# Optimization experiments

Hardware: AMD Instinct MI355X
Metric: run time of the kernel (lower is better)

The kernel has to match this reference:

```python
import jax, jax.numpy as jnp
import numpy as np

B, T, D = 2, 1024, 1024   # batch, timesteps (same for src/aux), model_dim
H, HD = 16, 64            # num_heads, head_dim (attention_dim = H*HD = 1024)
F = 4096                  # feedforward_dim
A = H * HD                # attention_dim
SCALE = float(HD) ** 0.5
LN_EPS = 1e-5
MASK_FILL = 1e-32         # faithful to masked_fill(1 - mask, 1e-32)


def setup_inputs() -> dict:
    key = jax.random.key(0)
    ks = jax.random.split(key, 12)
    def w(k, shape, fan):
        return jax.random.normal(k, shape, jnp.float32) / np.sqrt(fan)
    return {
        "src": jax.random.normal(ks[0], (B, T, D), jnp.float32),
        "aux": jax.random.normal(ks[1], (B, T, D), jnp.float32),
        "Wu": w(ks[2], (D, 3 * A), D), "bu": jnp.zeros((3 * A,), jnp.float32),
        "Wv": w(ks[3], (D, 3 * A), D), "bv": jnp.zeros((3 * A,), jnp.float32),
        "Wo": w(ks[4], (A, D), A),     "bo": jnp.zeros((D,), jnp.float32),
        "W1": w(ks[5], (D, F), D),     "b1": jnp.zeros((F,), jnp.float32),
        "W2": w(ks[6], (F, D), F),     "b2": jnp.zeros((D,), jnp.float32),
        "g1": jnp.ones((D,), jnp.float32), "be1": jnp.zeros((D,), jnp.float32),
        "g2": jnp.ones((D,), jnp.float32), "be2": jnp.zeros((D,), jnp.float32),
        "src_mask": jax.random.randint(ks[7], (B, T), 0, 2, jnp.int32),
        "aux_mask": jax.random.randint(ks[8], (B, T), 0, 2, jnp.int32),
    }


def _heads(x):
    # [B, T, A] -> [B, H, T, HD]
    b, t, _ = x.shape
    return x.reshape(b, t, H, HD).transpose(0, 2, 1, 3)


def _merge(x):
    # [B, H, T, HD] -> [B, T, A]
    b, h, t, hd = x.shape
    return x.transpose(0, 2, 1, 3).reshape(b, t, h * hd)


def _layernorm(x, g, b):
    m = jnp.mean(x, axis=-1, keepdims=True)
    v = jnp.var(x, axis=-1, keepdims=True)
    return (x - m) * jax.lax.rsqrt(v + LN_EPS) * g + b


def reference(src, aux, Wu, bu, Wv, bv, Wo, bo, W1, b1, W2, b2,
              g1, be1, g2, be2, src_mask, aux_mask):
    # dual-stream QKV projections
    q_u, k_u, v_u = (_heads(t) for t in jnp.split(src @ Wu + bu, 3, axis=-1))
    q_v, k_v, v_v = (_heads(t) for t in jnp.split(aux @ Wv + bv, 3, axis=-1))

    # masked scaled similarities (masked entries filled with 1e-32, per original)
    sim1 = jnp.einsum('bhqd,bhkd->bhqk', q_u / SCALE, k_v)        # [B,H,T1,T2]
    sim1 = jnp.where(aux_mask[:, None, None, :] > 0, sim1, MASK_FILL)
    sim2 = jnp.einsum('bhqd,bhkd->bhqk', q_v / SCALE, k_u)        # [B,H,T2,T1]
    sim2 = jnp.where(src_mask[:, None, None, :] > 0, sim2, MASK_FILL)

    # combined double-bmm attention
    comb_u = jnp.einsum('bhij,bhjk->bhik', sim1, sim2)            # [B,H,T1,T1]
    att_u = jax.nn.softmax(comb_u, axis=-1)
    out_u = _merge(jnp.einsum('bhqk,bhkd->bhqd', att_u, v_u)) @ Wo + bo

    comb_v = jnp.einsum('bhij,bhjk->bhik', sim2, sim1)            # [B,H,T2,T2]
    att_v = jax.nn.softmax(comb_v, axis=-1)
    out_v = _merge(jnp.einsum('bhqk,bhkd->bhqd', att_v, v_v)) @ Wo + bo

    def second_stage(x, attn):
        o1 = _layernorm(x + attn, g1, be1)
        ffn = jax.nn.relu(o1 @ W1 + b1) @ W2 + b2
        return _layernorm(o1 + ffn, g2, be2)

    return second_stage(src, out_u), second_stage(aux, out_v)
```

## Files before the change

### kernel.cpp

```cpp
#include <hip/hip_runtime.h>
#include <stdint.h>

typedef unsigned short u16;
typedef __attribute__((ext_vector_type(4))) float f32x4;
typedef __attribute__((ext_vector_type(8))) __bf16 bf16x8;
typedef __attribute__((ext_vector_type(8))) unsigned short u16x8;

#define T_ 1024
#define D_ 1024
#define HD_ 64

__device__ __forceinline__ float b2f(u16 u) {
    union { unsigned int i; float f; } x; x.i = ((unsigned int)u) << 16; return x.f;
}
__device__ __forceinline__ u16 f2b(float f) {
    union { float f; unsigned int i; } x; x.f = f;
    unsigned int i = x.i;
    unsigned int r = (i >> 16) & 1;
    i += 0x7fffu + r;
    return (u16)(i >> 16);
}

__device__ __forceinline__ void gl2lds16(const void* g, void* l) {
    auto gp = (const __attribute__((address_space(1))) unsigned int*)(unsigned long long)(g);
    auto lp = (__attribute__((address_space(3))) unsigned int*)(unsigned int)(unsigned long long)(l);
    __builtin_amdgcn_global_load_lds(gp, lp, 16, 0, 0);
}

__device__ __forceinline__ float wred_sum(float v) {
    #pragma unroll
    for (int o = 32; o > 0; o >>= 1) v += __shfl_down(v, o, 64);
    return v;
}
__device__ __forceinline__ float shx(float v, int m) { return __shfl_xor(v, m, 64); }

__global__ __launch_bounds__(256) void transpose_cvt(const float* __restrict__ in,
                                                     u16* __restrict__ out, int R, int C) {
    __shared__ float Ts[64][65];
    int c0 = blockIdx.x * 64, r0 = blockIdx.y * 64;
    int tid = threadIdx.x, tx = tid & 63, ty = tid >> 6;
    #pragma unroll
    for (int i = ty; i < 64; i += 4) Ts[i][tx] = in[(long)(r0 + i) * C + c0 + tx];
    __syncthreads();
    #pragma unroll
    for (int i = ty; i < 64; i += 4)
        out[(long)(c0 + i) * R + r0 + tx] = f2b(Ts[tx][i]);
}

__global__ __launch_bounds__(256) void transpose_split(const float* __restrict__ in,
                                                       u16* __restrict__ out, int R, int C) {
    __shared__ float Ts[64][65];
    int c0 = blockIdx.x * 64, r0 = blockIdx.y * 64;
    int tid = threadIdx.x, tx = tid & 63, ty = tid >> 6;
    #pragma unroll
    for (int i = ty; i < 64; i += 4) Ts[i][tx] = in[(long)(r0 + i) * C + c0 + tx];
    __syncthreads();
    #pragma unroll
    for (int i = ty; i < 64; i += 4) {
        float v = Ts[tx][i];
        u16 hi = f2b(v);
        u16 lo = f2b(v - b2f(hi));
        long base = (long)(c0 + i) * (3 * R) + r0 + tx;
        out[base] = hi;
        out[base + R] = hi;
        out[base + 2 * R] = lo;
    }
}

__global__ __launch_bounds__(256) void split_rows(const float* __restrict__ in,
                                                  u16* __restrict__ out) {
    long row = blockIdx.x;
    int tid = threadIdx.x;
    #pragma unroll
    for (int k = 0; k < 4; k++) {
        int c = tid + k * 256;
        float v = in[row * 1024 + c];
        u16 hi = f2b(v);
        u16 lo = f2b(v - b2f(hi));
        out[row * 3072 + c] = hi;
        out[row * 3072 + 1024 + c] = lo;
        out[row * 3072 + 2048 + c] = hi;
    }
}

enum { EPI_F32_BIAS = 0, EPI_BF16_BIAS = 1, EPI_BF16_BIAS_RELU = 2 };

template <int EPI, int BN>
__global__ __launch_bounds__(256) void gemm128(
    const u16* __restrict__ A, const u16* __restrict__ B, void* __restrict__ C,
    const float* __restrict__ bias,
    int M, int N, int K, int lda, int ldb, int ldc,
    long sAz, long sBz, long sCz) {
    __shared__ u16 As[2][128 * 32];
    __shared__ u16 Bs[2][BN * 32];
    const int tid = threadIdx.x, wave = tid >> 6, lane = tid & 63;
    const int m0 = blockIdx.x * 128, n0 = blockIdx.y * BN;
    const int z = blockIdx.z;
    const u16* Ab = A + (long)z * sAz;
    const u16* Bb = B + (long)z * sBz;
    const int srow = lane >> 2, scol = (lane & 3) * 8;
    constexpr int IT = (BN == 128) ? 4 : 2;
    f32x4 acc[IT][4];
    #pragma unroll
    for (int i = 0; i < IT; i++)
        #pragma unroll
        for (int j = 0; j < 4; j++) acc[i][j] = (f32x4){0.f, 0.f, 0.f, 0.f};
    const int wm = (BN == 128) ? (wave >> 1) * 64 : wave * 32;
    const int wn = (BN == 128) ? (wave & 1) * 64 : 0;
    const int fr = lane & 15, fk = (lane >> 4) * 8;

    {
        #pragma unroll
        for (int t = 0; t < 2; t++) {
            int rb = wave * 32 + t * 16;
            gl2lds16(Ab + (long)(m0 + rb + srow) * lda + scol, &As[0][rb * 32]);
        }
        if constexpr (BN == 128) {
            #pragma unroll
            for (int t = 0; t < 2; t++) {
                int rb = wave * 32 + t * 16;
                gl2lds16(Bb + (long)(n0 + rb + srow) * ldb + scol, &Bs[0][rb * 32]);
            }
        } else {
            int rb = wave * 16;
            gl2lds16(Bb + (long)(n0 + rb + srow) * ldb + scol, &Bs[0][rb * 32]);
        }
    }
    __syncthreads();

    for (int k0 = 0; k0 < K; k0 += 32) {
        const int buf = (k0 >> 5) & 1;
        const int kn = k0 + 32;
        if (kn < K) {
            #pragma unroll
            for (int t = 0; t < 2; t++) {
                int rb = wave * 32 + t * 16;
                gl2lds16(Ab + (long)(m0 + rb + srow) * lda + kn + scol, &As[buf ^ 1][rb * 32]);
            }
            if constexpr (BN == 128) {
                #pragma unroll
                for (int t = 0; t < 2; t++) {
                    int rb = wave * 32 + t * 16;
                    gl2lds16(Bb + (long)(n0 + rb + srow) * ldb + kn + scol, &Bs[buf ^ 1][rb * 32]);
                }
            } else {
                int rb = wave * 16;
                gl2lds16(Bb + (long)(n0 + rb + srow) * ldb + kn + scol, &Bs[buf ^ 1][rb * 32]);
            }
        }
        bf16x8 af[IT], bv[4];
        #pragma unroll
        for (int i = 0; i < IT; i++) af[i] = *(const bf16x8*)&As[buf][(wm + i * 16 + fr) * 32 + fk];
        #pragma unroll
        for (int j = 0; j < 4; j++) bv[j] = *(const bf16x8*)&Bs[buf][(wn + j * 16 + fr) * 32 + fk];
        #pragma unroll
        for (int i = 0; i < IT; i++)
            #pragma unroll
            for (int j = 0; j < 4; j++)
                acc[i][j] = __builtin_amdgcn_mfma_f32_16x16x32_bf16(af[i], bv[j], acc[i][j], 0, 0, 0);
        __syncthreads();
    }
    const int er = (lane >> 4) * 4, ec = lane & 15;
    #pragma unroll
    for (int i = 0; i < IT; i++)
        #pragma unroll
        for (int j = 0; j < 4; j++)
            #pragma unroll
            for (int r = 0; r < 4; r++) {
                const int gm = m0 + wm + i * 16 + er + r;
                const int gn = n0 + wn + j * 16 + ec;
                const float v = acc[i][j][r];
                if constexpr (EPI == EPI_F32_BIAS) {
                    ((float*)C)[(long)z * sCz + (long)gm * ldc + gn] = v + bias[gn];
                } else if constexpr (EPI == EPI_BF16_BIAS) {
                    ((u16*)C)[(long)z * sCz + (long)gm * ldc + gn] = f2b(v + bias[gn]);
                } else {
                    ((u16*)C)[(long)z * sCz + (long)gm * ldc + gn] = f2b(fmaxf(v + bias[gn], 0.0f));
                }
            }
}

__global__ __launch_bounds__(256) void repack_vt(const float* __restrict__ Uf,
                                                 const float* __restrict__ Vf,
                                                 u16* __restrict__ Vt) {
    __shared__ u16 Ts[64][65];
    int tid = threadIdx.x, tx = tid & 63, ty = tid >> 6;
    int t0 = blockIdx.x * 64;
    int sz = blockIdx.y, s = sz >> 5, z = sz & 31, b = z >> 4, h = z & 15;
    const float* srcp = s ? Vf : Uf;
    #pragma unroll
    for (int i = ty; i < 64; i += 4)
        Ts[i][tx] = f2b(srcp[(long)(b * T_ + t0 + i) * 3072 + 2048 + h * 64 + tx]);
    __syncthreads();
    u16* dst = Vt + (long)sz * HD_ * T_;
    #pragma unroll
    for (int i = ty; i < 64; i += 4) dst[(long)i * T_ + t0 + tx] = Ts[tx][i];
}

__global__ __launch_bounds__(256) void rs_part(const float* __restrict__ Uf,
                                               const float* __restrict__ Vf,
                                               const int* __restrict__ smask,
                                               const int* __restrict__ amask,
                                               float* __restrict__ RSp) {
    __shared__ float Ksh[64 * 64];
    __shared__ float Qsh[64 * 64];
    int idx = blockIdx.x;
    int mat = idx >> 5, z = idx & 31, b = z >> 4, h = z & 15;
    int chunk = blockIdx.y, j0 = chunk * 64;
    const float* base = mat ? Uf : Vf;
    const int* mk = mat ? smask : amask;
    int tid = threadIdx.x;
    float4* K4 = (float4*)Ksh;
    float4* Q4 = (float4*)Qsh;
    for (int ii = tid; ii < 1024; ii += 256) {
        int j = ii >> 4, d4 = ii & 15;
        long row = (long)(b * T_ + j0 + j) * 3072 + h * 64;
        int m = mk[b * T_ + j0 + j];
        float4 kv = ((const float4*)&base[row + 1024])[d4];
        if (m <= 0) kv = (float4){0.f, 0.f, 0.f, 0.f};
        K4[ii] = kv;
        Q4[ii] = ((const float4*)&base[row])[d4];
    }
    __syncthreads();
    int d1 = tid >> 2, c0 = (tid & 3) * 16;
    float4 a[4];
    #pragma unroll
    for (int k = 0; k < 4; k++) a[k] = (float4){0.f, 0.f, 0.f, 0.f};
    for (int j = 0; j < 64; j++) {
        float kv = Ksh[j * 64 + d1];
        const float4* q = (const float4*)&Qsh[j * 64 + c0];
        #pragma unroll
        for (int k = 0; k < 4; k++) {
            float4 qv = q[k];
            a[k].x += kv * qv.x; a[k].y += kv * qv.y;
            a[k].z += kv * qv.z; a[k].w += kv * qv.w;
        }
    }
    float4* out = (float4*)&RSp[((long)chunk * 64 + idx) * 4096 + d1 * 64 + c0];
    #pragma unroll
    for (int k = 0; k < 4; k++) out[k] = a[k];
}

__global__ __launch_bounds__(256) void rs_reduce(const float* __restrict__ RSp,
                                                 float* __restrict__ RS) {
    int gid = blockIdx.x * 256 + threadIdx.x;
    const float4* in = (const float4*)RSp;
    float4 s = (float4){0.f, 0.f, 0.f, 0.f};
    #pragma unroll
    for (int c = 0; c < 16; c++) {
        float4 v = in[(long)c * 65536 + gid];
        s.x += v.x; s.y += v.y; s.z += v.z; s.w += v.w;
    }
    ((float4*)RS)[gid] = s;
}

__global__ __launch_bounds__(256) void qprime(const float* __restrict__ Uf,
                                              const float* __restrict__ Vf,
                                              const float* __restrict__ RS,
                                              u16* __restrict__ Qs) {
    __shared__ float Rm[4096];
    __shared__ float Qsh[128][65];
    int t0 = blockIdx.x * 128;
    int sz = blockIdx.y, s = sz >> 5, z = sz & 31, b = z >> 4, h = z & 15;
    const float* Qf = s ? Vf : Uf;
    const float* mat = RS + (long)(s * 32 + z) * 4096;
    int tid = threadIdx.x;
    for (int ii = tid; ii < 1024; ii += 256)
        ((float4*)Rm)[ii] = ((const float4*)mat)[ii];
    for (int ii = tid; ii < 2048; ii += 256) {
        int j = ii >> 4, d4 = ii & 15;
        float4 v = ((const float4*)&Qf[(long)(b * T_ + t0 + j) * 3072 + h * 64])[d4];
        Qsh[j][d4 * 4] = v.x; Qsh[j][d4 * 4 + 1] = v.y;
        Qsh[j][d4 * 4 + 2] = v.z; Qsh[j][d4 * 4 + 3] = v.w;
    }
    __syncthreads();
    int r = tid >> 1, c0 = (tid & 1) * 32;
    float4 acc[8];
    #pragma unroll
    for (int k = 0; k < 8; k++) acc[k] = (float4){0.f, 0.f, 0.f, 0.f};
    for (int d1 = 0; d1 < 64; d1++) {
        float q = Qsh[r][d1];
        const float4* rm = (const float4*)&Rm[d1 * 64 + c0];
        #pragma unroll
        for (int k = 0; k < 8; k++) {
            float4 rv = rm[k];
            acc[k].x += q * rv.x; acc[k].y += q * rv.y;
            acc[k].z += q * rv.z; acc[k].w += q * rv.w;
        }
    }
    u16 hiA[32], loA[32];
    #pragma unroll
    for (int k = 0; k < 8; k++) {
        #pragma unroll
        for (int e = 0; e < 4; e++) {
            float x = ((const float*)&acc[k])[e] * (1.f / 64.f);
            int c = k * 4 + e;
            u16 hi = f2b(x);
            hiA[c] = hi;
            loA[c] = f2b(x - b2f(hi));
        }
    }
    u16* out = Qs + ((long)sz * T_ + (t0 + r)) * 128;
    #pragma unroll
    for (int i = 0; i < 4; i++) {
        *(u16x8*)&out[c0 + i * 8]      = *(const u16x8*)&hiA[i * 8];
        *(u16x8*)&out[64 + c0 + i * 8] = *(const u16x8*)&loA[i * 8];
    }
}

__global__ __launch_bounds__(256) void ksplit(const float* __restrict__ Uf,
                                              const float* __restrict__ Vf,
                                              const int* __restrict__ src_mask,
                                              const int* __restrict__ aux_mask,
                                              u16* __restrict__ Ks) {
    int t0 = blockIdx.x * 64;
    int sz = blockIdx.y, s = sz >> 5, z = sz & 31, b = z >> 4, h = z & 15;
    const float* Kf = s ? Vf : Uf;
    const int* mk = s ? aux_mask : src_mask;
    int tid = threadIdx.x;
    #pragma unroll
    for (int uu = 0; uu < 4; uu++) {
        int u = tid + uu * 256;
        int lr = u >> 4;
        int s16 = u & 15;
        int seg = s16 >> 3;
        int off = (s16 & 7) * 8;
        int r = t0 + lr;
        int m = mk[b * T_ + r];
        const float* srcp = &Kf[(long)(b * T_ + r) * 3072 + 1024 + h * 64 + off];
        float4 va = ((const float4*)srcp)[0];
        float4 vb = ((const float4*)srcp)[1];
        float xs[8] = {va.x, va.y, va.z, va.w, vb.x, vb.y, vb.z, vb.w};
        u16x8 wv;
        #pragma unroll
        for (int e = 0; e < 8; e++) {
            float x = (m > 0) ? xs[e] : 0.0f;
            u16 hi = f2b(x);
            wv[e] = (seg == 1) ? f2b(x - b2f(hi)) : hi;
        }
        *(u16x8*)&Ks[((long)sz * T_ + r) * 128 + seg * 64 + off] = wv;
    }
}

__global__ __launch_bounds__(512, 4) void flash_comb(const u16* __restrict__ Qs,
                                                     const u16* __restrict__ Ks,
                                                     const u16* __restrict__ Vt,
                                                     u16* __restrict__ ctx2) {
    __shared__ u16 Ksh[2][64 * 128];
    __shared__ u16 Vsh[2][64 * 64];
    __shared__ u16 Psh[128 * 64];
    const int tid = threadIdx.x, wave = tid >> 6, lane = tid & 63;
    const int z = blockIdx.x;
    const int m0 = blockIdx.y * 128;
    const int h = z & 15;
    const int g = lane >> 4, fr = lane & 15;
    const int wm = wave * 16;
    const u16* Qb = Qs + (long)z * T_ * 128;
    const u16* Kb = Ks + (long)z * T_ * 128;
    const u16* Vb = Vt + (long)z * HD_ * T_;

    auto STAGE = [&](int k0, int buf) {
        #pragma unroll
        for (int t = 0; t < 3; t++) {
            int slot = wave + t * 8;
            if (slot < 16) {
                int o16 = slot * 64 + lane;
                int row = o16 >> 4, c16 = o16 & 15;
                gl2lds16(Kb + (long)(k0 + row) * 128 + ((c16 ^ (row & 7)) * 8),
                         &Ksh[buf][slot * 512]);
            } else {
                int o16 = (slot - 16) * 64 + lane;
                int d = o16 >> 3, c16 = o16 & 7;
                gl2lds16(Vb + (long)d * T_ + k0 + ((c16 ^ (d & 7)) * 8),
                         &Vsh[buf][(slot - 16) * 512]);
            }
        }
    };

    bf16x8 qA[4];
    #pragma unroll
    for (int p = 0; p < 4; p++)
        qA[p] = *(const bf16x8*)&Qb[(long)(m0 + wm + fr) * 128 + p * 32 + g * 8];

    f32x4 oacc[4], mrun, lrun;
    mrun = (f32x4){-1e30f, -1e30f, -1e30f, -1e30f};
    lrun = (f32x4){0.f, 0.f, 0.f, 0.f};
    #pragma unroll
    for (int dj = 0; dj < 4; dj++) oacc[dj] = (f32x4){0.f, 0.f, 0.f, 0.f};

    STAGE(0, 0);
    __syncthreads();

    #pragma unroll 1
    for (int kt = 0; kt < 16; kt++) {
        const int buf = kt & 1;
        if (kt < 15) STAGE((kt + 1) * 64, buf ^ 1);

        f32x4 sacc[4];
        #pragma unroll
        for (int ki = 0; ki < 4; ki++) sacc[ki] = (f32x4){0.f, 0.f, 0.f, 0.f};
        __builtin_amdgcn_s_setprio(1);
        {
            bf16x8 kb[2][4];
            #pragma unroll
            for (int pk = 0; pk < 2; pk++)
                #pragma unroll
                for (int ki = 0; ki < 4; ki++) {
                    int row = ki * 16 + fr;
                    kb[pk][ki] = *(const bf16x8*)&Ksh[buf][row * 128 + (((pk * 4 + g) ^ (row & 7)) * 8)];
                }
            #pragma unroll
            for (int ki = 0; ki < 4; ki++) {
                sacc[ki] = __builtin_amdgcn_mfma_f32_16x16x32_bf16(qA[0], kb[0][ki], sacc[ki], 0, 0, 0);
                sacc[ki] = __builtin_amdgcn_mfma_f32_16x16x32_bf16(qA[1], kb[1][ki], sacc[ki], 0, 0, 0);
                sacc[ki] = __builtin_amdgcn_mfma_f32_16x16x32_bf16(qA[2], kb[0][ki], sacc[ki], 0, 0, 0);
                sacc[ki] = __builtin_amdgcn_mfma_f32_16x16x32_bf16(qA[3], kb[1][ki], sacc[ki], 0, 0, 0);
            }
            #pragma unroll
            for (int pk = 0; pk < 2; pk++)
                #pragma unroll
                for (int ki = 0; ki < 4; ki++) {
                    int row = ki * 16 + fr;
                    kb[pk][ki] = *(const bf16x8*)&Ksh[buf][row * 128 + ((((pk + 2) * 4 + g) ^ (row & 7)) * 8)];
                }
            #pragma unroll
            for (int ki = 0; ki < 4; ki++) {
                sacc[ki] = __builtin_amdgcn_mfma_f32_16x16x32_bf16(qA[0], kb[0][ki], sacc[ki], 0, 0, 0);
                sacc[ki] = __builtin_amdgcn_mfma_f32_16x16x32_bf16(qA[1], kb[1][ki], sacc[ki], 0, 0, 0);
            }
        }
        __builtin_amdgcn_s_setprio(0);

        f32x4 tm;
        #pragma unroll
        for (int e = 0; e < 4; e++)
            tm[e] = fmaxf(fmaxf(sacc[0][e], sacc[1][e]), fmaxf(sacc[2][e], sacc[3][e]));
        #pragma unroll
        for (int off = 1; off < 16; off <<= 1)
            #pragma unroll
            for (int e = 0; e < 4; e++) tm[e] = fmaxf(tm[e], shx(tm[e], off));

        int within = (tm[0] <= mrun[0] + 8.f) && (tm[1] <= mrun[1] + 8.f) &&
                     (tm[2] <= mrun[2] + 8.f) && (tm[3] <= mrun[3] + 8.f);
        if (!__all(within)) {
            f32x4 alpha;
            #pragma unroll
            for (int e = 0; e < 4; e++) {
                float mnew = fmaxf(mrun[e], tm[e]);
                alpha[e] = __expf(mrun[e] - mnew);
                mrun[e] = mnew;
            }
            #pragma unroll
            for (int dj = 0; dj < 4; dj++)
                #pragma unroll
                for (int e = 0; e < 4; e++) oacc[dj][e] *= alpha[e];
            #pragma unroll
            for (int e = 0; e < 4; e++) lrun[e] *= alpha[e];
        }

        f32x4 psum = (f32x4){0.f, 0.f, 0.f, 0.f};
        #pragma unroll
        for (int ki = 0; ki < 4; ki++) {
            #pragma unroll
            for (int e = 0; e < 4; e++) {
                float p = __expf(sacc[ki][e] - mrun[e]);
                psum[e] += p;
                int row = wm + g * 4 + e;
                Psh[row * 64 + ((ki * 16 + fr) ^ ((row & 7) << 3))] = f2b(p);
            }
        }
        #pragma unroll
        for (int off = 1; off < 16; off <<= 1)
            #pragma unroll
            for (int e = 0; e < 4; e++) psum[e] += shx(psum[e], off);
        #pragma unroll
        for (int e = 0; e < 4; e++) lrun[e] += psum[e];

        bf16x8 pa[2];
        #pragma unroll
        for (int ks = 0; ks < 2; ks++) {
            int row = wm + fr;
            pa[ks] = *(const bf16x8*)&Psh[row * 64 + (((ks * 4 + g) ^ (row & 7)) * 8)];
        }
        __builtin_amdgcn_s_setprio(1);
        #pragma unroll
        for (int dj = 0; dj < 4; dj++) {
            int d = dj * 16 + fr;
            bf16x8 vb0 = *(const bf16x8*)&Vsh[buf][d * 64 + (((0 * 4 + g) ^ (d & 7)) * 8)];
            bf16x8 vb1 = *(const bf16x8*)&Vsh[buf][d * 64 + (((1 * 4 + g) ^ (d & 7)) * 8)];
            oacc[dj] = __builtin_amdgcn_mfma_f32_16x16x32_bf16(pa[0], vb0, oacc[dj], 0, 0, 0);
            oacc[dj] = __builtin_amdgcn_mfma_f32_16x16x32_bf16(pa[1], vb1, oacc[dj], 0, 0, 0);
        }
        __builtin_amdgcn_s_setprio(0);
        __syncthreads();
    }

    f32x4 inv;
    #pragma unroll
    for (int e = 0; e < 4; e++) inv[e] = 1.f / lrun[e];
    #pragma unroll
    for (int dj = 0; dj < 4; dj++)
        #pragma unroll
        for (int e = 0; e < 4; e++) {
            int qr = m0 + wm + g * 4 + e;
            int dc = dj * 16 + fr;
            ctx2[((long)((z >> 4) * T_ + qr)) * D_ + h * 64 + dc] = f2b(oacc[dj][e] * inv[e]);
        }
}

template <bool XF32, bool OUTF32>
__global__ __launch_bounds__(256) void ln_fused2(const void* __restrict__ x0,
                                                 const void* __restrict__ x1,
                                                 const u16* __restrict__ y,
                                                 const float* __restrict__ g,
                                                 const float* __restrict__ be,
                                                 void* __restrict__ out) {
    __shared__ float red[8];
    int row = blockIdx.x;
    const void* xp = (row < 2048) ? x0 : x1;
    long xbase = (long)((row < 2048) ? row : row - 2048) * 1024;
    long base = (long)row * 1024;
    int tid = threadIdx.x, wave = tid >> 6, lane = tid & 63;
    float v[4];
    #pragma unroll
    for (int i = 0; i < 4; i++) {
        int c = tid + i * 256;
        float xv = XF32 ? ((const float*)xp)[xbase + c] : b2f(((const u16*)xp)[xbase + c]);
        v[i] = xv + b2f(y[base + c]);
    }
    float s = v[0] + v[1] + v[2] + v[3];
    float q = v[0] * v[0] + v[1] * v[1] + v[2] * v[2] + v[3] * v[3];
    s = wred_sum(s);
    q = wred_sum(q);
    if (lane == 0) { red[wave] = s; red[4 + wave] = q; }
    __syncthreads();
    s = red[0] + red[1] + red[2] + red[3];
    q = red[4] + red[5] + red[6] + red[7];
    float mean = s * (1.f / 1024.f);
    float var = q * (1.f / 1024.f) - mean * mean;
    float inv = rsqrtf(var + 1e-5f);
    #pragma unroll
    for (int i = 0; i < 4; i++) {
        int c = tid + i * 256;
        float o = (v[i] - mean) * inv * g[c] + be[c];
        if (OUTF32) ((float*)out)[base + c] = o;
        else ((u16*)out)[base + c] = f2b(o);
    }
}

extern "C" void kernel_launch(void* const* d_in, const int* in_sizes, int n_in,
                              void* d_out, int out_size, void* d_ws, size_t ws_size,
                              hipStream_t stream) {
    const float* src = (const float*)d_in[0];
    const float* aux = (const float*)d_in[1];
    const float* Wu = (const float*)d_in[2];
    const float* bu = (const float*)d_in[3];
    const float* Wv = (const float*)d_in[4];
    const float* bv = (const float*)d_in[5];
    const float* Wo = (const float*)d_in[6];
    const float* bo = (const float*)d_in[7];
    const float* W1 = (const float*)d_in[8];
    const float* b1 = (const float*)d_in[9];
    const float* W2 = (const float*)d_in[10];
    const float* b2 = (const float*)d_in[11];
    const float* g1 = (const float*)d_in[12];
    const float* be1 = (const float*)d_in[13];
    const float* g2 = (const float*)d_in[14];
    const float* be2 = (const float*)d_in[15];
    const int* src_mask = (const int*)d_in[16];
    const int* aux_mask = (const int*)d_in[17];

    char* w = (char*)d_ws;
    auto alloc = [&](size_t bytes) { char* p = w; w += (bytes + 255) & ~(size_t)255; return p; };
    u16* WoT = (u16*)alloc(1024L * 1024 * 2);
    u16* W1T = (u16*)alloc(4096L * 1024 * 2);
    u16* W2T = (u16*)alloc(1024L * 4096 * 2);
    u16* Vt  = (u16*)alloc(64L * 64 * 1024 * 2);
    float* RS = (float*)alloc(64L * 4096 * 4);
    u16* Qs = (u16*)alloc(64L * 1024 * 128 * 2);
    u16* Ks = (u16*)alloc(64L * 1024 * 128 * 2);
    char* scratch = (char*)alloc(84L * 1024 * 1024);
    u16* WS  = (u16*)(scratch);
    float* RSp = (float*)(scratch);
    u16* As_ = (u16*)(scratch + 18874368L);
    float* Uf = (float*)(scratch + 31457280L);
    float* Vf = (float*)(scratch + 56623104L);
    u16* ctx2   = (u16*)(scratch);
    u16* attn_s = (u16*)(scratch + 8388608L);
    u16* o1s    = (u16*)(scratch + 16777216L);
    u16* hbuf   = (u16*)(scratch + 25165824L);
    u16* fbuf   = (u16*)(scratch + 58720256L);

    transpose_cvt<<<dim3(16, 16), 256, 0, stream>>>(Wo, WoT, 1024, 1024);
    transpose_cvt<<<dim3(64, 16), 256, 0, stream>>>(W1, W1T, 1024, 4096);
    transpose_cvt<<<dim3(16, 64), 256, 0, stream>>>(W2, W2T, 4096, 1024);

    transpose_split<<<dim3(48, 16), 256, 0, stream>>>(Wu, WS, 1024, 3072);
    split_rows<<<2048, 256, 0, stream>>>(src, As_);
    gemm128<EPI_F32_BIAS, 128><<<dim3(16, 24, 1), 256, 0, stream>>>(
        As_, WS, Uf, bu, 2048, 3072, 3072, 3072, 3072, 3072, 0, 0, 0);
    transpose_split<<<dim3(48, 16), 256, 0, stream>>>(Wv, WS, 1024, 3072);
    split_rows<<<2048, 256, 0, stream>>>(aux, As_);
    gemm128<EPI_F32_BIAS, 128><<<dim3(16, 24, 1), 256, 0, stream>>>(
        As_, WS, Vf, bv, 2048, 3072, 3072, 3072, 3072, 3072, 0, 0, 0);
    repack_vt<<<dim3(16, 64), 256, 0, stream>>>(Uf, Vf, Vt);
    rs_part<<<dim3(64, 16), 256, 0, stream>>>(Uf, Vf, src_mask, aux_mask, RSp);
    rs_reduce<<<256, 256, 0, stream>>>(RSp, RS);
    qprime<<<dim3(8, 64), 256, 0, stream>>>(Uf, Vf, RS, Qs);
    ksplit<<<dim3(16, 64), 256, 0, stream>>>(Uf, Vf, src_mask, aux_mask, Ks);

    flash_comb<<<dim3(64, 8), 512, 0, stream>>>(Qs, Ks, Vt, ctx2);

    gemm128<EPI_BF16_BIAS, 64><<<dim3(16, 16, 2), 256, 0, stream>>>(
        ctx2, WoT, attn_s, bo, 2048, 1024, 1024, 1024, 1024, 1024,
        2048L * 1024, 0, 2048L * 1024);
    ln_fused2<true, false><<<4096, 256, 0, stream>>>(src, aux, attn_s, g1, be1, o1s);
    gemm128<EPI_BF16_BIAS_RELU, 128><<<dim3(16, 32, 2), 256, 0, stream>>>(
        o1s, W1T, hbuf, b1, 2048, 4096, 1024, 1024, 1024, 4096,
        2048L * 1024, 0, 2048L * 4096);
    gemm128<EPI_BF16_BIAS, 64><<<dim3(16, 16, 2), 256, 0, stream>>>(
        hbuf, W2T, fbuf, b2, 2048, 1024, 4096, 4096, 4096, 1024,
        2048L * 4096, 0, 2048L * 1024);
    ln_fused2<false, true><<<4096, 256, 0, stream>>>(o1s, o1s + 2048L * 1024, fbuf,
                                                     g2, be2, (float*)d_out);
}
```

Baseline: 540.9 us.

## Batch QKV projections into one split-bf16 GEMM with in-kernel hi/lo products

The two QKV projection GEMMs, which ran on K=3072 concatenated hi/lo operand layouts, are replaced by one batched kernel over both streams. Operands are stored once as hi|lo (K=2048), and each K-step issues three MFMAs (hi·hi, lo·hi, hi·lo) from shared memory with a swizzled layout. This removes the duplicated hi copies, shrinks the split buffers, and merges two launches into one larger grid. Accuracy is unchanged, at the cost of more registers per thread for the hi/lo fragments.

```diff
diff --git a/kernel.cpp b/kernel.cpp
--- a/kernel.cpp
+++ b/kernel.cpp
@@ -47,8 +47,8 @@
         out[(long)(c0 + i) * R + r0 + tx] = f2b(Ts[tx][i]);
 }
 
-__global__ __launch_bounds__(256) void transpose_split(const float* __restrict__ in,
-                                                       u16* __restrict__ out, int R, int C) {
+__global__ __launch_bounds__(256) void wsplit2(const float* __restrict__ in,
+                                               u16* __restrict__ out, int R, int C) {
     __shared__ float Ts[64][65];
     int c0 = blockIdx.x * 64, r0 = blockIdx.y * 64;
     int tid = threadIdx.x, tx = tid & 63, ty = tid >> 6;
@@ -60,16 +60,19 @@
         float v = Ts[tx][i];
         u16 hi = f2b(v);
         u16 lo = f2b(v - b2f(hi));
-        long base = (long)(c0 + i) * (3 * R) + r0 + tx;
+        long base = (long)(c0 + i) * (2 * R) + r0 + tx;
         out[base] = hi;
-        out[base + R] = hi;
-        out[base + 2 * R] = lo;
-    }
-}
-
-__global__ __launch_bounds__(256) void split_rows(const float* __restrict__ in,
-                                                  u16* __restrict__ out) {
+        out[base + R] = lo;
+    }
+}
+
+__global__ __launch_bounds__(256) void split2(const float* __restrict__ x0,
+                                              const float* __restrict__ x1,
+                                              u16* __restrict__ out) {
     long row = blockIdx.x;
+    int z = blockIdx.y;
+    const float* in = z ? x1 : x0;
+    u16* o = out + (long)z * 2048 * 2048;
     int tid = threadIdx.x;
     #pragma unroll
     for (int k = 0; k < 4; k++) {
@@ -77,9 +80,8 @@
         float v = in[row * 1024 + c];
         u16 hi = f2b(v);
         u16 lo = f2b(v - b2f(hi));
-        out[row * 3072 + c] = hi;
-        out[row * 3072 + 1024 + c] = lo;
-        out[row * 3072 + 2048 + c] = hi;
+        o[row * 2048 + c] = hi;
+        o[row * 2048 + 1024 + c] = lo;
     }
 }
 
@@ -177,6 +179,83 @@
                 } else {
                     ((u16*)C)[(long)z * sCz + (long)gm * ldc + gn] = f2b(fmaxf(v + bias[gn], 0.0f));
                 }
+            }
+}
+
+__global__ __launch_bounds__(256) void gemm_hl(
+    const u16* __restrict__ A, const u16* __restrict__ B, float* __restrict__ C,
+    const float* __restrict__ bias0, const float* __restrict__ bias1,
+    long sAz, long sBz, long sCz) {
+    __shared__ u16 As[2][128 * 64];
+    __shared__ u16 Bs[2][128 * 64];
+    const int tid = threadIdx.x, wave = tid >> 6, lane = tid & 63;
+    const int m0 = blockIdx.x * 128, n0 = blockIdx.y * 128;
+    const int z = blockIdx.z;
+    const u16* Ab = A + (long)z * sAz;
+    const u16* Bb = B + (long)z * sBz;
+    const float* bp = z ? bias1 : bias0;
+    const int fr = lane & 15, g = lane >> 4;
+    const int wm = (wave >> 1) * 64, wn = (wave & 1) * 64;
+    f32x4 acc[4][4];
+    #pragma unroll
+    for (int i = 0; i < 4; i++)
+        #pragma unroll
+        for (int j = 0; j < 4; j++) acc[i][j] = (f32x4){0.f, 0.f, 0.f, 0.f};
+
+    auto STAGE = [&](int k0, int buf) {
+        #pragma unroll
+        for (int t = 0; t < 8; t++) {
+            int slot = wave * 8 + t;
+            int o16 = (slot & 15) * 64 + lane;
+            int row = o16 >> 3, p = o16 & 7;
+            int l = p ^ (row & 7);
+            int srccol = (l < 4) ? (k0 + l * 8) : (1024 + k0 + (l - 4) * 8);
+            if (slot < 16)
+                gl2lds16(Ab + (long)(m0 + row) * 2048 + srccol, &As[buf][(slot & 15) * 512]);
+            else
+                gl2lds16(Bb + (long)(n0 + row) * 2048 + srccol, &Bs[buf][(slot & 15) * 512]);
+        }
+    };
+
+    STAGE(0, 0);
+    __syncthreads();
+
+    for (int k0 = 0; k0 < 1024; k0 += 32) {
+        const int buf = (k0 >> 5) & 1;
+        if (k0 + 32 < 1024) STAGE(k0 + 32, buf ^ 1);
+        bf16x8 ah[4], al[4], bh[4], bl[4];
+        #pragma unroll
+        for (int i = 0; i < 4; i++) {
+            int r = wm + i * 16 + fr;
+            ah[i] = *(const bf16x8*)&As[buf][r * 64 + ((g ^ (r & 7)) * 8)];
+            al[i] = *(const bf16x8*)&As[buf][r * 64 + (((4 + g) ^ (r & 7)) * 8)];
+        }
+        #pragma unroll
+        for (int j = 0; j < 4; j++) {
+            int r = wn + j * 16 + fr;
+            bh[j] = *(const bf16x8*)&Bs[buf][r * 64 + ((g ^ (r & 7)) * 8)];
+            bl[j] = *(const bf16x8*)&Bs[buf][r * 64 + (((4 + g) ^ (r & 7)) * 8)];
+        }
+        #pragma unroll
+        for (int i = 0; i < 4; i++)
+            #pragma unroll
+            for (int j = 0; j < 4; j++) {
+                acc[i][j] = __builtin_amdgcn_mfma_f32_16x16x32_bf16(ah[i], bh[j], acc[i][j], 0, 0, 0);
+                acc[i][j] = __builtin_amdgcn_mfma_f32_16x16x32_bf16(al[i], bh[j], acc[i][j], 0, 0, 0);
+                acc[i][j] = __builtin_amdgcn_mfma_f32_16x16x32_bf16(ah[i], bl[j], acc[i][j], 0, 0, 0);
+            }
+        __syncthreads();
+    }
+    const int er = (lane >> 4) * 4, ec = lane & 15;
+    #pragma unroll
+    for (int i = 0; i < 4; i++)
+        #pragma unroll
+        for (int j = 0; j < 4; j++)
+            #pragma unroll
+            for (int r = 0; r < 4; r++) {
+                const int gm = m0 + wm + i * 16 + er + r;
+                const int gn = n0 + wn + j * 16 + ec;
+                C[(long)z * sCz + (long)gm * 3072 + gn] = acc[i][j][r] + bp[gn];
             }
 }
 
@@ -579,12 +658,13 @@
     float* RS = (float*)alloc(64L * 4096 * 4);
     u16* Qs = (u16*)alloc(64L * 1024 * 128 * 2);
     u16* Ks = (u16*)alloc(64L * 1024 * 128 * 2);
-    char* scratch = (char*)alloc(84L * 1024 * 1024);
-    u16* WS  = (u16*)(scratch);
+    char* scratch = (char*)alloc(89L * 1024 * 1024);
+    u16* WS2 = (u16*)(scratch);
+    u16* As2 = (u16*)(scratch + 25165824L);
+    float* UVf = (float*)(scratch + 41943040L);
+    float* Uf = UVf;
+    float* Vf = UVf + 6291456L;
     float* RSp = (float*)(scratch);
-    u16* As_ = (u16*)(scratch + 18874368L);
-    float* Uf = (float*)(scratch + 31457280L);
-    float* Vf = (float*)(scratch + 56623104L);
     u16* ctx2   = (u16*)(scratch);
     u16* attn_s = (u16*)(scratch + 8388608L);
     u16* o1s    = (u16*)(scratch + 16777216L);
@@ -595,14 +675,11 @@
     transpose_cvt<<<dim3(64, 16), 256, 0, stream>>>(W1, W1T, 1024, 4096);
     transpose_cvt<<<dim3(16, 64), 256, 0, stream>>>(W2, W2T, 4096, 1024);
 
-    transpose_split<<<dim3(48, 16), 256, 0, stream>>>(Wu, WS, 1024, 3072);
-    split_rows<<<2048, 256, 0, stream>>>(src, As_);
-    gemm128<EPI_F32_BIAS, 128><<<dim3(16, 24, 1), 256, 0, stream>>>(
-        As_, WS, Uf, bu, 2048, 3072, 3072, 3072, 3072, 3072, 0, 0, 0);
-    transpose_split<<<dim3(48, 16), 256, 0, stream>>>(Wv, WS, 1024, 3072);
-    split_rows<<<2048, 256, 0, stream>>>(aux, As_);
-    gemm128<EPI_F32_BIAS, 128><<<dim3(16, 24, 1), 256, 0, stream>>>(
-        As_, WS, Vf, bv, 2048, 3072, 3072, 3072, 3072, 3072, 0, 0, 0);
+    wsplit2<<<dim3(48, 16), 256, 0, stream>>>(Wu, WS2, 1024, 3072);
+    wsplit2<<<dim3(48, 16), 256, 0, stream>>>(Wv, WS2 + 6291456L, 1024, 3072);
+    split2<<<dim3(2048, 2), 256, 0, stream>>>(src, aux, As2);
+    gemm_hl<<<dim3(16, 24, 2), 256, 0, stream>>>(
+        As2, WS2, UVf, bu, bv, 4194304L, 6291456L, 6291456L);
     repack_vt<<<dim3(16, 64), 256, 0, stream>>>(Uf, Vf, Vt);
     rs_part<<<dim3(64, 16), 256, 0, stream>>>(Uf, Vf, src_mask, aux_mask, RSp);
     rs_reduce<<<256, 256, 0, stream>>>(RSp, RS);
```

Result: faster. 508.6 us (-6.0%).
